# Performance work log

Hardware: AMD Instinct MI355X
Metric: run time of the kernel (lower is better)

Reference implementation:

```python
import jax, jax.numpy as jnp
import numpy as np

TOP_K = 6  # num_experts_per_tok


def _glu_mlp(x, wg, wu, wd):
    # DeepSeek MLP: down( silu(gate(x)) * up(x) )
    return (jax.nn.silu(x @ wg) * (x @ wu)) @ wd


def setup_inputs() -> dict:
    key = jax.random.key(0)
    ks = jax.random.split(key, 8)
    B, S, D, E, F, FS = 2, 2048, 1024, 8, 512, 1024
    sc = 0.02
    return {
        "hidden_states": jax.random.normal(ks[0], (B, S, D), jnp.float32),
        "router_w": jax.random.normal(ks[1], (D, E), jnp.float32) * sc,
        "w_gate": jax.random.normal(ks[2], (E, D, F), jnp.float32) * sc,
        "w_up": jax.random.normal(ks[3], (E, D, F), jnp.float32) * sc,
        "w_down": jax.random.normal(ks[4], (E, F, D), jnp.float32) * sc,
        "ws_gate": jax.random.normal(ks[5], (D, FS), jnp.float32) * sc,
        "ws_up": jax.random.normal(ks[6], (D, FS), jnp.float32) * sc,
        "ws_down": jax.random.normal(ks[7], (FS, D), jnp.float32) * sc,
    }


def reference(hidden_states, router_w, w_gate, w_up, w_down, ws_gate, ws_up, ws_down):
    B, S, D = hidden_states.shape
    x = hidden_states.reshape(-1, D)                       # [T, D] tokens
    # Gate: softmax router + top-k (DeepSeek gate, no renorm)
    scores = jax.nn.softmax(x @ router_w, axis=-1)         # [T, E]
    topk_w, topk_idx = jax.lax.top_k(scores, TOP_K)        # [T, K]
    # Expert SiLU-GLU MLPs evaluated for all experts (math-identical to the
    # argsort dispatch -> grouped GEMM -> scatter combine in moe_infer)
    g = jnp.einsum('td,edf->etf', x, w_gate)               # [E, T, F]
    u = jnp.einsum('td,edf->etf', x, w_up)                 # [E, T, F]
    f_all = jnp.einsum('etf,efd->ted', jax.nn.silu(g) * u, w_down)  # [T, E, D]
    # Combine: final[t] = sum_k topk_w[t,k] * expert_{topk_idx[t,k]}(x[t])
    picked = jnp.take_along_axis(f_all, topk_idx[:, :, None], axis=1)  # [T, K, D]
    y = jnp.sum(picked * topk_w[:, :, None], axis=1).reshape(B, S, D)
    # shared experts branch
    y = y + _glu_mlp(hidden_states, ws_gate, ws_up, ws_down)
    return y
```

## Files before the change

kernel.cpp:

```cpp
#include <hip/hip_runtime.h>

typedef __attribute__((ext_vector_type(8))) short bf16x8;
typedef __attribute__((ext_vector_type(4))) float floatx4;

static __device__ __forceinline__ float b2f(unsigned short u) {
  union { unsigned int i; float f; } v; v.i = ((unsigned int)u) << 16; return v.f;
}
static __device__ __forceinline__ unsigned short f2b(float f) {
  union { float f; unsigned int i; } v; v.f = f;
  unsigned int x = v.i;
  return (unsigned short)((x + 0x7fffu + ((x >> 16) & 1u)) >> 16);
}

#define GLDS(gp, lp) \
  __builtin_amdgcn_global_load_lds( \
      (const __attribute__((address_space(1))) unsigned int*)(gp), \
      (__attribute__((address_space(3))) unsigned int*)(lp), 16, 0, 0)

__global__ void cvt_f32_bf16(const float* __restrict__ src,
                             unsigned short* __restrict__ dst) {
  int i = (blockIdx.x * 256 + threadIdx.x) * 4;
  float4 v = *(const float4*)(src + i);
  ushort4 o;
  o.x = f2b(v.x); o.y = f2b(v.y); o.z = f2b(v.z); o.w = f2b(v.w);
  *(ushort4*)(dst + i) = o;
}

__global__ void transpose_f32_bf16(const float* __restrict__ src,
                                   unsigned short* __restrict__ dst, int K, int N) {
  __shared__ unsigned short tile[32][33];
  src += (size_t)blockIdx.z * K * N;
  dst += (size_t)blockIdx.z * K * N;
  const int bx = blockIdx.x * 32;
  const int by = blockIdx.y * 32;
  const int tx = threadIdx.x, ty = threadIdx.y;
#pragma unroll
  for (int i = 0; i < 4; i++)
    tile[ty + i * 8][tx] = f2b(src[(size_t)(by + ty + i * 8) * N + bx + tx]);
  __syncthreads();
#pragma unroll
  for (int i = 0; i < 4; i++)
    dst[(size_t)(bx + ty + i * 8) * K + by + tx] = tile[tx][ty + i * 8];
}

__global__ void router_topk(const float* __restrict__ X,
                            const float* __restrict__ RW,
                            float* __restrict__ cw) {
  const int t = blockIdx.x;
  const int lane = threadIdx.x;
  float acc[8];
#pragma unroll
  for (int e = 0; e < 8; e++) acc[e] = 0.f;
  for (int d = lane; d < 1024; d += 64) {
    float xv = X[(size_t)t * 1024 + d];
    const float* r = RW + d * 8;
    float4 r0 = *(const float4*)r;
    float4 r1 = *(const float4*)(r + 4);
    acc[0] += xv * r0.x; acc[1] += xv * r0.y;
    acc[2] += xv * r0.z; acc[3] += xv * r0.w;
    acc[4] += xv * r1.x; acc[5] += xv * r1.y;
    acc[6] += xv * r1.z; acc[7] += xv * r1.w;
  }
#pragma unroll
  for (int m = 1; m < 64; m <<= 1) {
#pragma unroll
    for (int e = 0; e < 8; e++) acc[e] += __shfl_xor(acc[e], m);
  }
  if (lane == 0) {
    float mx = acc[0];
#pragma unroll
    for (int e = 1; e < 8; e++) mx = fmaxf(mx, acc[e]);
    float prob[8], s = 0.f;
#pragma unroll
    for (int e = 0; e < 8; e++) { prob[e] = expf(acc[e] - mx); s += prob[e]; }
    float inv = 1.f / s;
#pragma unroll
    for (int e = 0; e < 8; e++) prob[e] *= inv;
    int m1 = 0;
#pragma unroll
    for (int e = 1; e < 8; e++) if (prob[e] < prob[m1]) m1 = e;
    int m2 = -1;
#pragma unroll
    for (int e = 0; e < 8; e++)
      if (e != m1 && (m2 < 0 || prob[e] < prob[m2])) m2 = e;
#pragma unroll
    for (int e = 0; e < 8; e++)
      cw[(size_t)t * 8 + e] = (e == m1 || e == m2) ? 0.f : prob[e];
  }
}

__global__ __launch_bounds__(256) void gemm_gu_fused(
    const unsigned short* __restrict__ X,
    const unsigned short* __restrict__ WgTe,
    const unsigned short* __restrict__ WgTs,
    const unsigned short* __restrict__ WuTe,
    const unsigned short* __restrict__ WuTs,
    unsigned short* __restrict__ H,
    const float* __restrict__ cw) {
  __shared__ __align__(16) unsigned short lA[128 * 32];
  __shared__ __align__(16) unsigned short lBg[64 * 32];
  __shared__ __align__(16) unsigned short lBu[64 * 32];
  const int tid = threadIdx.x;
  const int wid = tid >> 6, lane = tid & 63;
  const int lr = lane & 15, quad = lane >> 4;
  const int wm = wid >> 1, wn = wid & 1;
  const int m0 = blockIdx.x * 128;
  const int n0 = blockIdx.y * 64;

  const unsigned short *Bg, *Bu;
  int eidx = -1;
  if (n0 < 4096) {
    eidx = n0 >> 9;
    size_t off = ((size_t)eidx * 512 + (n0 & 511)) * 1024;
    Bg = WgTe + off; Bu = WuTe + off;
  } else {
    size_t off = (size_t)(n0 - 4096) * 1024;
    Bg = WgTs + off; Bu = WuTs + off;
  }

  floatx4 ag[4][2], au[4][2];
#pragma unroll
  for (int i = 0; i < 4; i++)
#pragma unroll
    for (int j = 0; j < 2; j++) { ag[i][j] = (floatx4)0.f; au[i][j] = (floatx4)0.f; }

  for (int k0 = 0; k0 < 1024; k0 += 32) {
    __syncthreads();
    {
#pragma unroll
      for (int i = 0; i < 2; i++) {
        int c = i * 256 + tid;
        int row = c >> 2;
        int g = ((c & 3) ^ ((row >> 1) & 3)) << 3;
        GLDS(X + (size_t)(m0 + row) * 1024 + k0 + g,
             lA + (size_t)(i * 256 + wid * 64) * 8);
      }
      int c = tid;
      int row = c >> 2;
      int g = ((c & 3) ^ ((row >> 1) & 3)) << 3;
      GLDS(Bg + (size_t)row * 1024 + k0 + g, lBg + (size_t)(wid * 64) * 8);
      GLDS(Bu + (size_t)row * 1024 + k0 + g, lBu + (size_t)(wid * 64) * 8);
    }
    __syncthreads();
    bf16x8 af[4], bg[2], bu[2];
#pragma unroll
    for (int mt = 0; mt < 4; mt++) {
      int row = wm * 64 + mt * 16 + lr;
      af[mt] = *(const bf16x8*)(lA + row * 32 + ((quad ^ ((row >> 1) & 3)) << 3));
    }
#pragma unroll
    for (int nt = 0; nt < 2; nt++) {
      int row = wn * 32 + nt * 16 + lr;
      int o = row * 32 + ((quad ^ ((row >> 1) & 3)) << 3);
      bg[nt] = *(const bf16x8*)(lBg + o);
      bu[nt] = *(const bf16x8*)(lBu + o);
    }
#pragma unroll
    for (int mt = 0; mt < 4; mt++)
#pragma unroll
      for (int nt = 0; nt < 2; nt++) {
        ag[mt][nt] = __builtin_amdgcn_mfma_f32_16x16x32_bf16(
            af[mt], bg[nt], ag[mt][nt], 0, 0, 0);
        au[mt][nt] = __builtin_amdgcn_mfma_f32_16x16x32_bf16(
            af[mt], bu[nt], au[mt][nt], 0, 0, 0);
      }
  }

#pragma unroll
  for (int mt = 0; mt < 4; mt++) {
#pragma unroll
    for (int nt = 0; nt < 2; nt++) {
#pragma unroll
      for (int r = 0; r < 4; r++) {
        int row = m0 + wm * 64 + mt * 16 + quad * 4 + r;
        int col = n0 + wn * 32 + nt * 16 + lr;
        float g = ag[mt][nt][r];
        float u = au[mt][nt][r];
        float s = (eidx >= 0) ? cw[(size_t)row * 8 + eidx] : 1.0f;
        float silu = g / (1.0f + __expf(-g));
        H[(size_t)row * 5120 + col] = f2b(s * silu * u);
      }
    }
  }
}

__global__ __launch_bounds__(256) void gemm_down(
    const unsigned short* __restrict__ H,
    const unsigned short* __restrict__ WdTe,
    const unsigned short* __restrict__ WdTs,
    float* __restrict__ Y) {
  __shared__ __align__(16) unsigned short lA[128 * 64];
  __shared__ __align__(16) unsigned short lB[64 * 64];
  const int tid = threadIdx.x;
  const int wid = tid >> 6, lane = tid & 63;
  const int lr = lane & 15, quad = lane >> 4;
  const int wm = wid >> 1, wn = wid & 1;
  const int m0 = blockIdx.x * 128;
  const int n0 = blockIdx.y * 64;

  floatx4 acc[4][2];
#pragma unroll
  for (int i = 0; i < 4; i++)
#pragma unroll
    for (int j = 0; j < 2; j++) acc[i][j] = (floatx4)0.f;

  for (int k0 = 0; k0 < 5120; k0 += 64) {
    __syncthreads();
#pragma unroll
    for (int i = 0; i < 4; i++) {
      int c = i * 256 + tid;
      int row = c >> 3;
      int g = ((c & 7) ^ (row & 7)) << 3;
      GLDS(H + (size_t)(m0 + row) * 5120 + k0 + g,
           lA + (size_t)(i * 256 + wid * 64) * 8);
    }
#pragma unroll
    for (int i = 0; i < 2; i++) {
      int c = i * 256 + tid;
      int row = c >> 3;
      int g = ((c & 7) ^ (row & 7)) << 3;
      const unsigned short* gpb;
      if (k0 < 4096) {
        gpb = WdTe + (size_t)(k0 >> 9) * (1024 * 512) +
              (size_t)(n0 + row) * 512 + (k0 & 511) + g;
      } else {
        gpb = WdTs + (size_t)(n0 + row) * 1024 + (k0 - 4096) + g;
      }
      GLDS(gpb, lB + (size_t)(i * 256 + wid * 64) * 8);
    }
    __syncthreads();
    bf16x8 af[4][2], bfr[2][2];
#pragma unroll
    for (int mt = 0; mt < 4; mt++) {
      int row = wm * 64 + mt * 16 + lr;
#pragma unroll
      for (int kt = 0; kt < 2; kt++)
        af[mt][kt] = *(const bf16x8*)(lA + row * 64 +
                                      ((((kt << 2) + quad) ^ (row & 7)) << 3));
    }
#pragma unroll
    for (int nt = 0; nt < 2; nt++) {
      int row = wn * 32 + nt * 16 + lr;
#pragma unroll
      for (int kt = 0; kt < 2; kt++)
        bfr[nt][kt] = *(const bf16x8*)(lB + row * 64 +
                                       ((((kt << 2) + quad) ^ (row & 7)) << 3));
    }
#pragma unroll
    for (int kt = 0; kt < 2; kt++)
#pragma unroll
      for (int mt = 0; mt < 4; mt++)
#pragma unroll
        for (int nt = 0; nt < 2; nt++)
          acc[mt][nt] = __builtin_amdgcn_mfma_f32_16x16x32_bf16(
              af[mt][kt], bfr[nt][kt], acc[mt][nt], 0, 0, 0);
  }

#pragma unroll
  for (int mt = 0; mt < 4; mt++)
#pragma unroll
    for (int nt = 0; nt < 2; nt++)
#pragma unroll
      for (int r = 0; r < 4; r++) {
        int row = m0 + wm * 64 + mt * 16 + quad * 4 + r;
        int col = n0 + wn * 32 + nt * 16 + lr;
        Y[(size_t)row * 1024 + col] = acc[mt][nt][r];
      }
}

extern "C" void kernel_launch(void* const* d_in, const int* in_sizes, int n_in,
                              void* d_out, int out_size, void* d_ws, size_t ws_size,
                              hipStream_t stream) {
  const float* hs  = (const float*)d_in[0];
  const float* rw  = (const float*)d_in[1];
  const float* wg  = (const float*)d_in[2];
  const float* wu  = (const float*)d_in[3];
  const float* wd  = (const float*)d_in[4];
  const float* wsg = (const float*)d_in[5];
  const float* wsu = (const float*)d_in[6];
  const float* wsd = (const float*)d_in[7];
  float* out = (float*)d_out;

  char* p = (char*)d_ws;
  float* cw = (float*)p;                    p += (size_t)4096 * 8 * 4;
  unsigned short* Xb   = (unsigned short*)p; p += (size_t)4096 * 1024 * 2;
  unsigned short* wgT  = (unsigned short*)p; p += (size_t)8 * 512 * 1024 * 2;
  unsigned short* wuT  = (unsigned short*)p; p += (size_t)8 * 512 * 1024 * 2;
  unsigned short* wsgT = (unsigned short*)p; p += (size_t)1024 * 1024 * 2;
  unsigned short* wsuT = (unsigned short*)p; p += (size_t)1024 * 1024 * 2;
  unsigned short* wdT  = (unsigned short*)p; p += (size_t)8 * 1024 * 512 * 2;
  unsigned short* wsdT = (unsigned short*)p; p += (size_t)1024 * 1024 * 2;
  unsigned short* GH   = (unsigned short*)p;
  const size_t base_bytes = (size_t)(p - (char*)d_ws);

  int chunks = 8;
  for (int c = 1; c <= 8; c *= 2) {
    size_t gh_bytes = ((size_t)4096 / c) * 5120 * 2;
    if (base_bytes + gh_bytes <= ws_size) { chunks = c; break; }
  }
  const int rows = 4096 / chunks;

  dim3 tb(32, 8);
  cvt_f32_bf16<<<4096, 256, 0, stream>>>(hs, Xb);
  router_topk<<<4096, 64, 0, stream>>>(hs, rw, cw);
  transpose_f32_bf16<<<dim3(16, 32, 8), tb, 0, stream>>>(wg, wgT, 1024, 512);
  transpose_f32_bf16<<<dim3(16, 32, 8), tb, 0, stream>>>(wu, wuT, 1024, 512);
  transpose_f32_bf16<<<dim3(32, 16, 8), tb, 0, stream>>>(wd, wdT, 512, 1024);
  transpose_f32_bf16<<<dim3(32, 32, 1), tb, 0, stream>>>(wsg, wsgT, 1024, 1024);
  transpose_f32_bf16<<<dim3(32, 32, 1), tb, 0, stream>>>(wsu, wsuT, 1024, 1024);
  transpose_f32_bf16<<<dim3(32, 32, 1), tb, 0, stream>>>(wsd, wsdT, 1024, 1024);

  for (int c = 0; c < chunks; c++) {
    const unsigned short* Xc = Xb + (size_t)c * rows * 1024;
    const float* cwc = cw + (size_t)c * rows * 8;
    float* outc = out + (size_t)c * rows * 1024;
    gemm_gu_fused<<<dim3(rows / 128, 80), 256, 0, stream>>>(
        Xc, wgT, wsgT, wuT, wsuT, GH, cwc);
    gemm_down<<<dim3(rows / 128, 16), 256, 0, stream>>>(GH, wdT, wsdT, outc);
  }
}
```

Measured before the change: 317.3 us.

## Swizzle GEMM block order across XCDs and merge weight transpose launches

GEMM blocks now use a flattened 1D grid, and a swizzle maps each block so that blocks sharing the same N-column weight strip land on different XCDs while covering consecutive M tiles. The aim is better L2 reuse of weight tiles on the multi-XCD MI355X. Separately, the six weight transpose/convert launches are merged into three (gate+up together, down, and the three shared weights together), which reduces launch overhead. The index arithmetic adds a little cost per block, and the fallback path is used when Mb is not a multiple of 8.

```diff
diff --git a/kernel.cpp b/kernel.cpp
--- a/kernel.cpp
+++ b/kernel.cpp
@@ -16,6 +16,20 @@
   __builtin_amdgcn_global_load_lds( \
       (const __attribute__((address_space(1))) unsigned int*)(gp), \
       (__attribute__((address_space(3))) unsigned int*)(lp), 16, 0, 0)
+
+static __device__ __forceinline__ void swizzle_mn(int lin, int Mb, int Nb,
+                                                  int& m_idx, int& n_idx) {
+  if ((Mb & 7) == 0) {
+    int xcd = lin & 7;
+    int idx = lin >> 3;
+    int nstrips = Mb >> 3;
+    m_idx = (idx % nstrips) * 8 + xcd;
+    n_idx = idx / nstrips;
+  } else {
+    m_idx = lin % Mb;
+    n_idx = lin / Mb;
+  }
+}
 
 __global__ void cvt_f32_bf16(const float* __restrict__ src,
                              unsigned short* __restrict__ dst) {
@@ -26,11 +40,17 @@
   *(ushort4*)(dst + i) = o;
 }
 
-__global__ void transpose_f32_bf16(const float* __restrict__ src,
-                                   unsigned short* __restrict__ dst, int K, int N) {
+__global__ void transpose_f32_bf16_2(const float* __restrict__ sA,
+                                     unsigned short* __restrict__ dA, int nzA,
+                                     const float* __restrict__ sB,
+                                     unsigned short* __restrict__ dB,
+                                     int K, int N) {
   __shared__ unsigned short tile[32][33];
-  src += (size_t)blockIdx.z * K * N;
-  dst += (size_t)blockIdx.z * K * N;
+  int z = blockIdx.z;
+  const float* src;
+  unsigned short* dst;
+  if (z < nzA) { src = sA + (size_t)z * K * N; dst = dA + (size_t)z * K * N; }
+  else { src = sB + (size_t)(z - nzA) * K * N; dst = dB + (size_t)(z - nzA) * K * N; }
   const int bx = blockIdx.x * 32;
   const int by = blockIdx.y * 32;
   const int tx = threadIdx.x, ty = threadIdx.y;
@@ -41,6 +61,27 @@
 #pragma unroll
   for (int i = 0; i < 4; i++)
     dst[(size_t)(bx + ty + i * 8) * K + by + tx] = tile[tx][ty + i * 8];
+}
+
+__global__ void transpose3_1024(const float* __restrict__ s0,
+                                const float* __restrict__ s1,
+                                const float* __restrict__ s2,
+                                unsigned short* __restrict__ d0,
+                                unsigned short* __restrict__ d1,
+                                unsigned short* __restrict__ d2) {
+  __shared__ unsigned short tile[32][33];
+  const float* src = (blockIdx.z == 0) ? s0 : (blockIdx.z == 1) ? s1 : s2;
+  unsigned short* dst = (blockIdx.z == 0) ? d0 : (blockIdx.z == 1) ? d1 : d2;
+  const int bx = blockIdx.x * 32;
+  const int by = blockIdx.y * 32;
+  const int tx = threadIdx.x, ty = threadIdx.y;
+#pragma unroll
+  for (int i = 0; i < 4; i++)
+    tile[ty + i * 8][tx] = f2b(src[(size_t)(by + ty + i * 8) * 1024 + bx + tx]);
+  __syncthreads();
+#pragma unroll
+  for (int i = 0; i < 4; i++)
+    dst[(size_t)(bx + ty + i * 8) * 1024 + by + tx] = tile[tx][ty + i * 8];
 }
 
 __global__ void router_topk(const float* __restrict__ X,
@@ -96,7 +137,7 @@
     const unsigned short* __restrict__ WuTe,
     const unsigned short* __restrict__ WuTs,
     unsigned short* __restrict__ H,
-    const float* __restrict__ cw) {
+    const float* __restrict__ cw, int Mb) {
   __shared__ __align__(16) unsigned short lA[128 * 32];
   __shared__ __align__(16) unsigned short lBg[64 * 32];
   __shared__ __align__(16) unsigned short lBu[64 * 32];
@@ -104,8 +145,10 @@
   const int wid = tid >> 6, lane = tid & 63;
   const int lr = lane & 15, quad = lane >> 4;
   const int wm = wid >> 1, wn = wid & 1;
-  const int m0 = blockIdx.x * 128;
-  const int n0 = blockIdx.y * 64;
+  int m_idx, n_idx;
+  swizzle_mn(blockIdx.x, Mb, 80, m_idx, n_idx);
+  const int m0 = m_idx * 128;
+  const int n0 = n_idx * 64;
 
   const unsigned short *Bg, *Bu;
   int eidx = -1;
@@ -188,15 +231,17 @@
     const unsigned short* __restrict__ H,
     const unsigned short* __restrict__ WdTe,
     const unsigned short* __restrict__ WdTs,
-    float* __restrict__ Y) {
+    float* __restrict__ Y, int Mb) {
   __shared__ __align__(16) unsigned short lA[128 * 64];
   __shared__ __align__(16) unsigned short lB[64 * 64];
   const int tid = threadIdx.x;
   const int wid = tid >> 6, lane = tid & 63;
   const int lr = lane & 15, quad = lane >> 4;
   const int wm = wid >> 1, wn = wid & 1;
-  const int m0 = blockIdx.x * 128;
-  const int n0 = blockIdx.y * 64;
+  int m_idx, n_idx;
+  swizzle_mn(blockIdx.x, Mb, 16, m_idx, n_idx);
+  const int m0 = m_idx * 128;
+  const int n0 = n_idx * 64;
 
   floatx4 acc[4][2];
 #pragma unroll
@@ -299,23 +344,24 @@
     if (base_bytes + gh_bytes <= ws_size) { chunks = c; break; }
   }
   const int rows = 4096 / chunks;
+  const int Mb = rows / 128;
 
   dim3 tb(32, 8);
   cvt_f32_bf16<<<4096, 256, 0, stream>>>(hs, Xb);
   router_topk<<<4096, 64, 0, stream>>>(hs, rw, cw);
-  transpose_f32_bf16<<<dim3(16, 32, 8), tb, 0, stream>>>(wg, wgT, 1024, 512);
-  transpose_f32_bf16<<<dim3(16, 32, 8), tb, 0, stream>>>(wu, wuT, 1024, 512);
-  transpose_f32_bf16<<<dim3(32, 16, 8), tb, 0, stream>>>(wd, wdT, 512, 1024);
-  transpose_f32_bf16<<<dim3(32, 32, 1), tb, 0, stream>>>(wsg, wsgT, 1024, 1024);
-  transpose_f32_bf16<<<dim3(32, 32, 1), tb, 0, stream>>>(wsu, wsuT, 1024, 1024);
-  transpose_f32_bf16<<<dim3(32, 32, 1), tb, 0, stream>>>(wsd, wsdT, 1024, 1024);
+  transpose_f32_bf16_2<<<dim3(16, 32, 16), tb, 0, stream>>>(
+      wg, wgT, 8, wu, wuT, 1024, 512);
+  transpose_f32_bf16_2<<<dim3(32, 16, 8), tb, 0, stream>>>(
+      wd, wdT, 8, wd, wdT, 512, 1024);
+  transpose3_1024<<<dim3(32, 32, 3), tb, 0, stream>>>(
+      wsg, wsu, wsd, wsgT, wsuT, wsdT);
 
   for (int c = 0; c < chunks; c++) {
     const unsigned short* Xc = Xb + (size_t)c * rows * 1024;
     const float* cwc = cw + (size_t)c * rows * 8;
     float* outc = out + (size_t)c * rows * 1024;
-    gemm_gu_fused<<<dim3(rows / 128, 80), 256, 0, stream>>>(
-        Xc, wgT, wsgT, wuT, wsuT, GH, cwc);
-    gemm_down<<<dim3(rows / 128, 16), 256, 0, stream>>>(GH, wdT, wsdT, outc);
-  }
-}
+    gemm_gu_fused<<<Mb * 80, 256, 0, stream>>>(
+        Xc, wgT, wsgT, wuT, wsuT, GH, cwc, Mb);
+    gemm_down<<<Mb * 16, 256, 0, stream>>>(GH, wdT, wsdT, outc, Mb);
+  }
+}
```

Result: no change. 313.0 us (-1.4%).
